# Kernel tuning notes

Hardware: AMD Instinct MI355X
Metric: run time of the kernel (lower is better)

## Reference

```python
import jax, jax.numpy as jnp
import numpy as np

B, S, D = 4, 2048, 512
H, DQK, DV = 6, 64, 64
PROJ = (DQK + DQK + DV) * H  # 1152
EPS = 1e-5


def setup_inputs() -> dict:
    key = jax.random.key(0)
    ks = jax.random.split(key, 5)
    sc = 0.05
    return {
        "x": jax.random.normal(ks[0], (B, S, D), jnp.float32),
        "Wp": jax.random.normal(ks[1], (PROJ, D), jnp.float32) * sc,
        "bp": jax.random.normal(ks[2], (PROJ,), jnp.float32) * sc,
        "Wo": jax.random.normal(ks[3], (D, H * DV), jnp.float32) * sc,
        "bo": jax.random.normal(ks[4], (D,), jnp.float32) * sc,
        "gamma": jnp.ones((D,), jnp.float32),
        "beta": jnp.zeros((D,), jnp.float32),
    }


def reference(x, Wp, bp, Wo, bo, gamma, beta):
    b, s, d = x.shape
    # 1x1 Conv1d projection == pointwise linear: [b,s,d] @ [d,proj] -> [b,s,proj]
    proj = jnp.einsum("bsd,pd->bsp", x, Wp) + bp
    q, k, v = proj[..., : H * DQK], proj[..., H * DQK : 2 * H * DQK], proj[..., 2 * H * DQK :]
    # split heads -> [b,h,s,depth]
    q = q.reshape(b, s, H, DQK).transpose(0, 2, 1, 3)
    k = k.reshape(b, s, H, DQK).transpose(0, 2, 1, 3)
    v = v.reshape(b, s, H, DV).transpose(0, 2, 1, 3)
    scores = jnp.einsum("bhqd,bhkd->bhqk", q, k) / jnp.sqrt(jnp.float32(DQK))
    attn = jax.nn.softmax(scores, axis=-1)  # softmax over kv axis
    out = jnp.einsum("bhqk,bhkd->bhqd", attn, v)
    # concat heads -> [b,s,h*dv]
    concat = out.transpose(0, 2, 1, 3).reshape(b, s, H * DV)
    y = jnp.einsum("bsf,df->bsd", concat, Wo) + bo
    z = x + y
    mu = jnp.mean(z, axis=-1, keepdims=True)
    var = jnp.mean(jnp.square(z - mu), axis=-1, keepdims=True)
    return (z - mu) / jnp.sqrt(var + EPS) * gamma + beta
```

## Files before the change

kernel.cpp:

```cpp
#include <hip/hip_runtime.h>

typedef __bf16 bf16;
typedef __bf16 bf16x8 __attribute__((ext_vector_type(8)));
typedef __bf16 bf16x4 __attribute__((ext_vector_type(4)));
typedef float  f32x4  __attribute__((ext_vector_type(4)));

#define BB 4
#define SS 2048
#define DD 512
#define HH 6
#define DH 64
#define PROJ 1152
#define FF 384
#define LDK 72

__device__ __forceinline__ bool probe_fp32(const unsigned* p) {
    return p[0] == 0x3F800000u;
}

struct CvtSrcs { const void* s[7]; };

#define CB0 524288
#define CB1 598016
#define CB2 622592
#define CB3 622736
#define CB4 622800
#define CB5 622864
#define CB6 622928

__global__ __launch_bounds__(256) void cvt_all_kernel(
    CvtSrcs srcs, bf16* __restrict__ dst, const unsigned* __restrict__ probe)
{
    const int t = blockIdx.x * 256 + threadIdx.x;
    if (t >= CB6) return;
    int seg, base;
    if      (t < CB0) { seg = 0; base = 0;   }
    else if (t < CB1) { seg = 1; base = CB0; }
    else if (t < CB2) { seg = 2; base = CB1; }
    else if (t < CB3) { seg = 3; base = CB2; }
    else if (t < CB4) { seg = 4; base = CB3; }
    else if (t < CB5) { seg = 5; base = CB4; }
    else              { seg = 6; base = CB5; }
    const int li = (t - base) * 8;
    if (probe_fp32(probe)) {
        const float* s = (const float*)srcs.s[seg] + li;
        bf16x8 o;
#pragma unroll
        for (int j = 0; j < 8; ++j) o[j] = (bf16)s[j];
        *(bf16x8*)&dst[(size_t)t * 8] = o;
    } else {
        *(bf16x8*)&dst[(size_t)t * 8] =
            *(const bf16x8*)((const bf16*)srcs.s[seg] + li);
    }
}

template<int MERGE, int STORE_F32>
__global__ __launch_bounds__(256) void gemm_bt_kernel(
    const bf16* __restrict__ A, const float* __restrict__ lpart,
    const bf16* __restrict__ B, const bf16* __restrict__ bias,
    void* __restrict__ Cout, int M, int N, int K)
{
    __shared__ __attribute__((aligned(16))) bf16 sA[128 * LDK];
    __shared__ __attribute__((aligned(16))) bf16 sB[128 * LDK];

    const int tid  = threadIdx.x;
    const int lane = tid & 63;
    const int wave = tid >> 6;
    const int wm = (wave >> 1) * 64;
    const int wn = (wave & 1) * 64;
    const int l15 = lane & 15;
    const int quad = lane >> 4;
    const int bm = blockIdx.x * 128;
    const int bn = blockIdx.y * 128;
    const int KT = K / 64;

    int srow[4], scol;
    scol = (tid & 7) << 3;
#pragma unroll
    for (int j = 0; j < 4; ++j) srow[j] = (j * 256 + tid) >> 3;

    const bf16* pA[4]; const bf16* pB[4];
    const float* pl0[4];
#pragma unroll
    for (int j = 0; j < 4; ++j) {
        if (MERGE) {
            int row = bm + srow[j];
            int b = row >> 11, q = row & (SS - 1);
            pA[j]  = A + ((size_t)(b * HH) * SS + q) * DH + scol;
            pl0[j] = lpart + (size_t)(b * HH) * SS + q;
        } else {
            pA[j] = A + (size_t)(bm + srow[j]) * K + scol;
        }
        pB[j] = B + (size_t)(bn + srow[j]) * K + scol;
    }

    bf16x8 ar0[4], ar1[4], br[4];
    float li0[4], li1[4];
#pragma unroll
    for (int j = 0; j < 4; ++j) {
        ar0[j] = *(const bf16x8*)pA[j];
        if (MERGE) {
            ar1[j] = *(const bf16x8*)(pA[j] + (size_t)BB * HH * SS * DH);
            li0[j] = pl0[j][0];
            li1[j] = pl0[j][(size_t)BB * HH * SS];
        }
        br[j] = *(const bf16x8*)pB[j];
    }

    const f32x4 fzero = {0.f, 0.f, 0.f, 0.f};
    f32x4 acc[4][4];
#pragma unroll
    for (int mi = 0; mi < 4; ++mi)
#pragma unroll
        for (int ni = 0; ni < 4; ++ni) acc[mi][ni] = fzero;

    for (int kt = 0; kt < KT; ++kt) {
        __syncthreads();
#pragma unroll
        for (int j = 0; j < 4; ++j) {
            if (MERGE) {
                float inv = 1.f / (li0[j] + li1[j]);
                bf16x8 m;
#pragma unroll
                for (int e = 0; e < 8; ++e)
                    m[e] = (bf16)(((float)ar0[j][e] + (float)ar1[j][e]) * inv);
                *(bf16x8*)&sA[srow[j] * LDK + scol] = m;
            } else {
                *(bf16x8*)&sA[srow[j] * LDK + scol] = ar0[j];
            }
            *(bf16x8*)&sB[srow[j] * LDK + scol] = br[j];
        }
        __syncthreads();

        if (kt + 1 < KT) {
#pragma unroll
            for (int j = 0; j < 4; ++j) {
                if (MERGE) {
                    pA[j]  += (size_t)SS * DH;
                    pl0[j] += SS;
                    ar0[j] = *(const bf16x8*)pA[j];
                    ar1[j] = *(const bf16x8*)(pA[j] + (size_t)BB * HH * SS * DH);
                    li0[j] = pl0[j][0];
                    li1[j] = pl0[j][(size_t)BB * HH * SS];
                } else {
                    pA[j] += 64;
                    ar0[j] = *(const bf16x8*)pA[j];
                }
                pB[j] += 64;
                br[j] = *(const bf16x8*)pB[j];
            }
        }

#pragma unroll
        for (int kk = 0; kk < 2; ++kk) {
            bf16x8 af[4], bfr[4];
#pragma unroll
            for (int i = 0; i < 4; ++i) {
                af[i]  = *(const bf16x8*)&sA[(wm + i * 16 + l15) * LDK + kk * 32 + quad * 8];
                bfr[i] = *(const bf16x8*)&sB[(wn + i * 16 + l15) * LDK + kk * 32 + quad * 8];
            }
#pragma unroll
            for (int mi = 0; mi < 4; ++mi)
#pragma unroll
                for (int ni = 0; ni < 4; ++ni)
                    acc[mi][ni] = __builtin_amdgcn_mfma_f32_16x16x32_bf16(
                        af[mi], bfr[ni], acc[mi][ni], 0, 0, 0);
        }
    }

#pragma unroll
    for (int mi = 0; mi < 4; ++mi) {
        int row = bm + wm + mi * 16 + quad * 4;
#pragma unroll
        for (int ni = 0; ni < 4; ++ni) {
            int col = bn + wn + ni * 16 + l15;
            float bv = (float)bias[col];
#pragma unroll
            for (int r = 0; r < 4; ++r) {
                float v = acc[mi][ni][r] + bv;
                if (STORE_F32) ((float*)Cout)[(size_t)(row + r) * N + col] = v;
                else           ((bf16*)Cout)[(size_t)(row + r) * N + col] = (bf16)v;
            }
        }
    }
}

__global__ __launch_bounds__(256) void vt_kernel(
    const bf16* __restrict__ proj, bf16* __restrict__ Vt)
{
    __shared__ __attribute__((aligned(16))) bf16 lt[64 * LDK];

    const int tid = threadIdx.x;
    const int s0 = blockIdx.x * 64;
    const int bh = blockIdx.y;
    const int b = bh / HH, h = bh % HH;

#pragma unroll
    for (int i = 0; i < 2; ++i) {
        int vid = i * 256 + tid;
        int sl = vid >> 3;
        int dc = (vid & 7) << 3;
        bf16x8 v = *(const bf16x8*)&proj[
            (size_t)(b * SS + s0 + sl) * PROJ + 2 * HH * DH + h * DH + dc];
#pragma unroll
        for (int j = 0; j < 8; ++j) {
            int d = dc + j;
            lt[d * LDK + (sl ^ (((d >> 3) & 3) * 8))] = v[j];
        }
    }
    __syncthreads();

#pragma unroll
    for (int i = 0; i < 2; ++i) {
        int vid = i * 256 + tid;
        int d = vid >> 3;
        int sc = (vid & 7) << 3;
        bf16x8 v = *(const bf16x8*)&lt[d * LDK + (sc ^ (((d >> 3) & 3) * 8))];
        *(bf16x8*)&Vt[(size_t)bh * DH * SS + (size_t)d * SS + s0 + sc] = v;
    }
}

__global__ __launch_bounds__(256) void attn_kernel(
    const bf16* __restrict__ proj, const bf16* __restrict__ Vt,
    bf16* __restrict__ Opart, float* __restrict__ lpart)
{
    __shared__ __attribute__((aligned(16))) bf16 sK [64 * LDK];
    __shared__ __attribute__((aligned(16))) bf16 sVt[64 * LDK];
    __shared__ __attribute__((aligned(16))) bf16 sP [4 * 32 * LDK];

    const int tid  = threadIdx.x;
    const int lane = tid & 63;
    const int wave = tid >> 6;
    const int l15  = lane & 15;
    const int quad = lane >> 4;

    const int bh = blockIdx.y;
    const int b = bh / HH, h = bh % HH;
    const int q0 = blockIdx.x * 128;
    const int kz = blockIdx.z;
    const bf16* base = proj + (size_t)b * SS * PROJ;
    const bf16* vtb  = Vt + (size_t)bh * DH * SS;

    const int sr = tid >> 3;
    const int sc = (tid & 7) << 3;

    bf16x8 qf[2][2];
#pragma unroll
    for (int g = 0; g < 2; ++g) {
        const int qrow = q0 + wave * 32 + g * 16 + l15;
#pragma unroll
        for (int ks = 0; ks < 2; ++ks) {
            qf[ks][g] = *(const bf16x8*)&base[
                (size_t)qrow * PROJ + h * DH + ks * 32 + quad * 8];
#pragma unroll
            for (int j = 0; j < 8; ++j)
                qf[ks][g][j] = (bf16)((float)qf[ks][g][j] * 0.125f);
        }
    }

    const f32x4 fzero = {0.f, 0.f, 0.f, 0.f};
    float l_part[2] = {0.f, 0.f};
    f32x4 oacc[2][4];
#pragma unroll
    for (int g = 0; g < 2; ++g)
#pragma unroll
        for (int fi = 0; fi < 4; ++fi) oacc[g][fi] = fzero;

    bf16* pw = &sP[wave * 32 * LDK];

    const int kt0 = kz * (SS / 128);
    const int kt1 = kt0 + SS / 128;

    bf16x8 kreg[2], vreg[2];
#pragma unroll
    for (int i = 0; i < 2; ++i) {
        int r = i * 32 + sr;
        kreg[i] = *(const bf16x8*)&base[(size_t)(kt0 * 64 + r) * PROJ + HH * DH + h * DH + sc];
        vreg[i] = *(const bf16x8*)&vtb[(size_t)r * SS + kt0 * 64 + sc];
    }

    for (int kt = kt0; kt < kt1; ++kt) {
        __syncthreads();
#pragma unroll
        for (int i = 0; i < 2; ++i) {
            int r = i * 32 + sr;
            *(bf16x8*)&sK [r * LDK + sc] = kreg[i];
            *(bf16x8*)&sVt[r * LDK + sc] = vreg[i];
        }
        __syncthreads();
        if (kt + 1 < kt1) {
#pragma unroll
            for (int i = 0; i < 2; ++i) {
                int r = i * 32 + sr;
                kreg[i] = *(const bf16x8*)&base[
                    (size_t)((kt + 1) * 64 + r) * PROJ + HH * DH + h * DH + sc];
                vreg[i] = *(const bf16x8*)&vtb[(size_t)r * SS + (kt + 1) * 64 + sc];
            }
        }

        f32x4 st[2][4];
#pragma unroll
        for (int g = 0; g < 2; ++g)
#pragma unroll
            for (int mi = 0; mi < 4; ++mi) st[g][mi] = fzero;
#pragma unroll
        for (int ks = 0; ks < 2; ++ks)
#pragma unroll
            for (int mi = 0; mi < 4; ++mi) {
                bf16x8 af = *(const bf16x8*)&sK[(mi * 16 + l15) * LDK + ks * 32 + quad * 8];
#pragma unroll
                for (int g = 0; g < 2; ++g)
                    st[g][mi] = __builtin_amdgcn_mfma_f32_16x16x32_bf16(
                        af, qf[ks][g], st[g][mi], 0, 0, 0);
            }

#pragma unroll
        for (int g = 0; g < 2; ++g)
#pragma unroll
            for (int mi = 0; mi < 4; ++mi)
#pragma unroll
                for (int r = 0; r < 4; ++r) {
                    st[g][mi][r] = __expf(st[g][mi][r]);
                    l_part[g] += st[g][mi][r];
                }

#pragma unroll
        for (int g = 0; g < 2; ++g)
#pragma unroll
            for (int mi = 0; mi < 4; ++mi) {
                bf16x4 p4;
#pragma unroll
                for (int r = 0; r < 4; ++r) p4[r] = (bf16)st[g][mi][r];
                *(bf16x4*)&pw[(g * 16 + l15) * LDK + mi * 16 + quad * 4] = p4;
            }

#pragma unroll
        for (int ks = 0; ks < 2; ++ks) {
            bf16x8 bfrag[2];
#pragma unroll
            for (int g = 0; g < 2; ++g)
                bfrag[g] = *(const bf16x8*)&pw[(g * 16 + l15) * LDK + ks * 32 + quad * 8];
#pragma unroll
            for (int fi = 0; fi < 4; ++fi) {
                bf16x8 af = *(const bf16x8*)&sVt[(fi * 16 + l15) * LDK + ks * 32 + quad * 8];
#pragma unroll
                for (int g = 0; g < 2; ++g)
                    oacc[g][fi] = __builtin_amdgcn_mfma_f32_16x16x32_bf16(
                        af, bfrag[g], oacc[g][fi], 0, 0, 0);
            }
        }
    }

#pragma unroll
    for (int g = 0; g < 2; ++g) {
        l_part[g] += __shfl_xor(l_part[g], 16);
        l_part[g] += __shfl_xor(l_part[g], 32);
    }

    const size_t zoff = (size_t)(kz * BB * HH + bh) * SS;
#pragma unroll
    for (int g = 0; g < 2; ++g) {
        const int qg = q0 + wave * 32 + g * 16 + l15;
        bf16* orow = Opart + (zoff + qg) * DH;
#pragma unroll
        for (int fi = 0; fi < 4; ++fi) {
            bf16x4 o4;
#pragma unroll
            for (int r = 0; r < 4; ++r) o4[r] = (bf16)oacc[g][fi][r];
            *(bf16x4*)&orow[fi * 16 + quad * 4] = o4;
        }
    }
    if (lane < 16) {
#pragma unroll
        for (int g = 0; g < 2; ++g)
            lpart[zoff + q0 + wave * 32 + g * 16 + lane] = l_part[g];
    }
}

__global__ __launch_bounds__(256) void ln_kernel(
    const void* __restrict__ xr, const float* __restrict__ y,
    const bf16* __restrict__ gamma, const bf16* __restrict__ beta,
    void* __restrict__ out, const unsigned* __restrict__ probe)
{
    const bool f32 = probe_fp32(probe);
    const int lane = threadIdx.x & 63;
    const int wave = threadIdx.x >> 6;
    const int row = blockIdx.x * 4 + wave;
    const size_t off = (size_t)row * DD + lane * 8;

    float z[8];
    if (f32) {
        const float* xf = (const float*)xr;
#pragma unroll
        for (int j = 0; j < 8; ++j) z[j] = xf[off + j];
    } else {
        bf16x8 xv = *(const bf16x8*)&((const bf16*)xr)[off];
#pragma unroll
        for (int j = 0; j < 8; ++j) z[j] = (float)xv[j];
    }
    f32x4 y0 = *(const f32x4*)&y[off];
    f32x4 y1 = *(const f32x4*)&y[off + 4];
#pragma unroll
    for (int j = 0; j < 4; ++j) { z[j] += y0[j]; z[j + 4] += y1[j]; }

    float s = 0.f;
#pragma unroll
    for (int j = 0; j < 8; ++j) s += z[j];
#pragma unroll
    for (int m = 1; m < 64; m <<= 1) s += __shfl_xor(s, m);
    float mu = s * (1.f / DD);
    float s2 = 0.f;
#pragma unroll
    for (int j = 0; j < 8; ++j) { float d = z[j] - mu; s2 += d * d; }
#pragma unroll
    for (int m = 1; m < 64; m <<= 1) s2 += __shfl_xor(s2, m);
    float rs = rsqrtf(s2 * (1.f / DD) + 1e-5f);

    bf16x8 gm = *(const bf16x8*)&gamma[lane * 8];
    bf16x8 be = *(const bf16x8*)&beta[lane * 8];
    if (f32) {
        f32x4 o0, o1;
#pragma unroll
        for (int j = 0; j < 4; ++j) {
            o0[j] = (z[j]     - mu) * rs * (float)gm[j]     + (float)be[j];
            o1[j] = (z[j + 4] - mu) * rs * (float)gm[j + 4] + (float)be[j + 4];
        }
        *(f32x4*)&((float*)out)[off]     = o0;
        *(f32x4*)&((float*)out)[off + 4] = o1;
    } else {
        bf16x8 o;
#pragma unroll
        for (int j = 0; j < 8; ++j)
            o[j] = (bf16)((z[j] - mu) * rs * (float)gm[j] + (float)be[j]);
        *(bf16x8*)&((bf16*)out)[off] = o;
    }
}

extern "C" void kernel_launch(void* const* d_in, const int* in_sizes, int n_in,
                              void* d_out, int out_size, void* d_ws, size_t ws_size,
                              hipStream_t stream)
{
    const unsigned* probe = (const unsigned*)d_in[5];

    char* ws = (char*)d_ws;
    size_t o = 0;
    bf16* xb   = (bf16*)(ws + o); o += (size_t)BB * SS * DD * 2;
    bf16* Wpb  = (bf16*)(ws + o); o += (size_t)PROJ * DD * 2;
    bf16* Wob  = (bf16*)(ws + o); o += (size_t)DD * FF * 2;
    bf16* bpb  = (bf16*)(ws + o); o += PROJ * 2;
    bf16* bob  = (bf16*)(ws + o); o += DD * 2;
    bf16* gb   = (bf16*)(ws + o); o += DD * 2;
    bf16* bb   = (bf16*)(ws + o); o += DD * 2;
    bf16* proj = (bf16*)(ws + o); o += (size_t)BB * SS * PROJ * 2;
    bf16* vtbuf  = (bf16*)(ws + o); o += (size_t)BB * HH * DH * SS * 2;
    bf16* Opart  = (bf16*)(ws + o); o += (size_t)2 * BB * HH * SS * DH * 2;
    float* lpart = (float*)(ws + o); o += (size_t)2 * BB * HH * SS * 4;
    float* ybuf = (float*)proj;

    CvtSrcs srcs;
    srcs.s[0] = d_in[0]; srcs.s[1] = d_in[1]; srcs.s[2] = d_in[3];
    srcs.s[3] = d_in[2]; srcs.s[4] = d_in[4]; srcs.s[5] = d_in[5];
    srcs.s[6] = d_in[6];
    cvt_all_kernel<<<(CB6 + 255) / 256, 256, 0, stream>>>(srcs, xb, probe);

    gemm_bt_kernel<0, 0><<<dim3((BB * SS) / 128, PROJ / 128), 256, 0, stream>>>(
        xb, nullptr, Wpb, bpb, proj, BB * SS, PROJ, DD);
    vt_kernel<<<dim3(SS / 64, BB * HH), 256, 0, stream>>>(proj, vtbuf);
    attn_kernel<<<dim3(SS / 128, BB * HH, 2), 256, 0, stream>>>(
        proj, vtbuf, Opart, lpart);
    gemm_bt_kernel<1, 1><<<dim3((BB * SS) / 128, DD / 128), 256, 0, stream>>>(
        Opart, lpart, Wob, bob, ybuf, BB * SS, DD, FF);
    ln_kernel<<<dim3((BB * SS) / 4), 256, 0, stream>>>(
        d_in[0], ybuf, gb, bb, d_out, probe);
}
```

Measured before the change: 166.7 us.

## Double-buffer global prefetch two tiles ahead and use exp2 with folded log2e scale

Both the GEMM and attention kernels now keep two register sets of prefetched tiles and issue global loads two k-steps ahead, so more load latency is hidden behind MFMA work. The attention softmax folds log2(e) into the Q scale and uses the hardware exp2 instruction. It also accumulates row sums as vector adds rather than scalar chains. This costs extra registers, which may lower occupancy, and assumes the k-tile count is even.

```diff
diff --git a/kernel.cpp b/kernel.cpp
--- a/kernel.cpp
+++ b/kernel.cpp
@@ -16,6 +16,14 @@
 
 __device__ __forceinline__ bool probe_fp32(const unsigned* p) {
     return p[0] == 0x3F800000u;
+}
+
+__device__ __forceinline__ float fast_exp2(float x) {
+#if __has_builtin(__builtin_amdgcn_exp2f)
+    return __builtin_amdgcn_exp2f(x);
+#else
+    return __expf(x * 0.69314718f);
+#endif
 }
 
 struct CvtSrcs { const void* s[7]; };
@@ -74,8 +82,8 @@
     const int bn = blockIdx.y * 128;
     const int KT = K / 64;
 
-    int srow[4], scol;
-    scol = (tid & 7) << 3;
+    int srow[4];
+    const int scol = (tid & 7) << 3;
 #pragma unroll
     for (int j = 0; j < 4; ++j) srow[j] = (j * 256 + tid) >> 3;
 
@@ -94,18 +102,29 @@
         pB[j] = B + (size_t)(bn + srow[j]) * K + scol;
     }
 
-    bf16x8 ar0[4], ar1[4], br[4];
-    float li0[4], li1[4];
-#pragma unroll
-    for (int j = 0; j < 4; ++j) {
-        ar0[j] = *(const bf16x8*)pA[j];
-        if (MERGE) {
-            ar1[j] = *(const bf16x8*)(pA[j] + (size_t)BB * HH * SS * DH);
-            li0[j] = pl0[j][0];
-            li1[j] = pl0[j][(size_t)BB * HH * SS];
-        }
-        br[j] = *(const bf16x8*)pB[j];
-    }
+    auto loadAB = [&](bf16x8 (&a0)[4], bf16x8 (&a1)[4],
+                      float (&l0)[4], float (&l1)[4], bf16x8 (&b)[4]) {
+#pragma unroll
+        for (int j = 0; j < 4; ++j) {
+            a0[j] = *(const bf16x8*)pA[j];
+            if (MERGE) {
+                a1[j] = *(const bf16x8*)(pA[j] + (size_t)BB * HH * SS * DH);
+                l0[j] = pl0[j][0];
+                l1[j] = pl0[j][(size_t)BB * HH * SS];
+                pA[j]  += (size_t)SS * DH;
+                pl0[j] += SS;
+            } else {
+                pA[j] += 64;
+            }
+            b[j] = *(const bf16x8*)pB[j];
+            pB[j] += 64;
+        }
+    };
+
+    bf16x8 a0A[4], a1A[4], bA[4]; float l0A[4], l1A[4];
+    bf16x8 a0B[4], a1B[4], bB[4]; float l0B[4], l1B[4];
+    loadAB(a0A, a1A, l0A, l1A, bA);
+    loadAB(a0B, a1B, l0B, l1B, bB);
 
     const f32x4 fzero = {0.f, 0.f, 0.f, 0.f};
     f32x4 acc[4][4];
@@ -114,42 +133,25 @@
 #pragma unroll
         for (int ni = 0; ni < 4; ++ni) acc[mi][ni] = fzero;
 
-    for (int kt = 0; kt < KT; ++kt) {
+    auto step = [&](int kt, bf16x8 (&a0)[4], bf16x8 (&a1)[4],
+                    float (&l0)[4], float (&l1)[4], bf16x8 (&b)[4]) {
         __syncthreads();
 #pragma unroll
         for (int j = 0; j < 4; ++j) {
             if (MERGE) {
-                float inv = 1.f / (li0[j] + li1[j]);
+                float inv = 1.f / (l0[j] + l1[j]);
                 bf16x8 m;
 #pragma unroll
                 for (int e = 0; e < 8; ++e)
-                    m[e] = (bf16)(((float)ar0[j][e] + (float)ar1[j][e]) * inv);
+                    m[e] = (bf16)(((float)a0[j][e] + (float)a1[j][e]) * inv);
                 *(bf16x8*)&sA[srow[j] * LDK + scol] = m;
             } else {
-                *(bf16x8*)&sA[srow[j] * LDK + scol] = ar0[j];
-            }
-            *(bf16x8*)&sB[srow[j] * LDK + scol] = br[j];
+                *(bf16x8*)&sA[srow[j] * LDK + scol] = a0[j];
+            }
+            *(bf16x8*)&sB[srow[j] * LDK + scol] = b[j];
         }
         __syncthreads();
-
-        if (kt + 1 < KT) {
-#pragma unroll
-            for (int j = 0; j < 4; ++j) {
-                if (MERGE) {
-                    pA[j]  += (size_t)SS * DH;
-                    pl0[j] += SS;
-                    ar0[j] = *(const bf16x8*)pA[j];
-                    ar1[j] = *(const bf16x8*)(pA[j] + (size_t)BB * HH * SS * DH);
-                    li0[j] = pl0[j][0];
-                    li1[j] = pl0[j][(size_t)BB * HH * SS];
-                } else {
-                    pA[j] += 64;
-                    ar0[j] = *(const bf16x8*)pA[j];
-                }
-                pB[j] += 64;
-                br[j] = *(const bf16x8*)pB[j];
-            }
-        }
+        if (kt + 2 < KT) loadAB(a0, a1, l0, l1, b);
 
 #pragma unroll
         for (int kk = 0; kk < 2; ++kk) {
@@ -166,6 +168,11 @@
                     acc[mi][ni] = __builtin_amdgcn_mfma_f32_16x16x32_bf16(
                         af[mi], bfr[ni], acc[mi][ni], 0, 0, 0);
         }
+    };
+
+    for (int kt = 0; kt < KT; kt += 2) {
+        step(kt,     a0A, a1A, l0A, l1A, bA);
+        step(kt + 1, a0B, a1B, l0B, l1B, bB);
     }
 
 #pragma unroll
@@ -244,6 +251,7 @@
     const int sr = tid >> 3;
     const int sc = (tid & 7) << 3;
 
+    const float QS = 0.18033688f;
     bf16x8 qf[2][2];
 #pragma unroll
     for (int g = 0; g < 2; ++g) {
@@ -254,12 +262,12 @@
                 (size_t)qrow * PROJ + h * DH + ks * 32 + quad * 8];
 #pragma unroll
             for (int j = 0; j < 8; ++j)
-                qf[ks][g][j] = (bf16)((float)qf[ks][g][j] * 0.125f);
+                qf[ks][g][j] = (bf16)((float)qf[ks][g][j] * QS);
         }
     }
 
     const f32x4 fzero = {0.f, 0.f, 0.f, 0.f};
-    float l_part[2] = {0.f, 0.f};
+    f32x4 lacc[2] = {fzero, fzero};
     f32x4 oacc[2][4];
 #pragma unroll
     for (int g = 0; g < 2; ++g)
@@ -271,58 +279,61 @@
     const int kt0 = kz * (SS / 128);
     const int kt1 = kt0 + SS / 128;
 
-    bf16x8 kreg[2], vreg[2];
+    const bf16* pk[2]; const bf16* pv[2];
 #pragma unroll
     for (int i = 0; i < 2; ++i) {
         int r = i * 32 + sr;
-        kreg[i] = *(const bf16x8*)&base[(size_t)(kt0 * 64 + r) * PROJ + HH * DH + h * DH + sc];
-        vreg[i] = *(const bf16x8*)&vtb[(size_t)r * SS + kt0 * 64 + sc];
-    }
-
-    for (int kt = kt0; kt < kt1; ++kt) {
+        pk[i] = &base[(size_t)(kt0 * 64 + r) * PROJ + HH * DH + h * DH + sc];
+        pv[i] = &vtb[(size_t)r * SS + kt0 * 64 + sc];
+    }
+    auto loadKV = [&](bf16x8 (&kr)[2], bf16x8 (&vr)[2]) {
+#pragma unroll
+        for (int i = 0; i < 2; ++i) {
+            kr[i] = *(const bf16x8*)pk[i];
+            vr[i] = *(const bf16x8*)pv[i];
+            pk[i] += (size_t)64 * PROJ;
+            pv[i] += 64;
+        }
+    };
+
+    bf16x8 kA[2], vA[2], kB[2], vB[2];
+    loadKV(kA, vA);
+    loadKV(kB, vB);
+
+    auto tile = [&](int kt, bf16x8 (&kr)[2], bf16x8 (&vr)[2]) {
         __syncthreads();
 #pragma unroll
         for (int i = 0; i < 2; ++i) {
             int r = i * 32 + sr;
-            *(bf16x8*)&sK [r * LDK + sc] = kreg[i];
-            *(bf16x8*)&sVt[r * LDK + sc] = vreg[i];
+            *(bf16x8*)&sK [r * LDK + sc] = kr[i];
+            *(bf16x8*)&sVt[r * LDK + sc] = vr[i];
         }
         __syncthreads();
-        if (kt + 1 < kt1) {
-#pragma unroll
-            for (int i = 0; i < 2; ++i) {
-                int r = i * 32 + sr;
-                kreg[i] = *(const bf16x8*)&base[
-                    (size_t)((kt + 1) * 64 + r) * PROJ + HH * DH + h * DH + sc];
-                vreg[i] = *(const bf16x8*)&vtb[(size_t)r * SS + (kt + 1) * 64 + sc];
-            }
-        }
+        if (kt + 2 < kt1) loadKV(kr, vr);
 
         f32x4 st[2][4];
 #pragma unroll
+        for (int mi = 0; mi < 4; ++mi) {
+            bf16x8 af0 = *(const bf16x8*)&sK[(mi * 16 + l15) * LDK + quad * 8];
+            bf16x8 af1 = *(const bf16x8*)&sK[(mi * 16 + l15) * LDK + 32 + quad * 8];
+#pragma unroll
+            for (int g = 0; g < 2; ++g) {
+                st[g][mi] = __builtin_amdgcn_mfma_f32_16x16x32_bf16(
+                    af0, qf[0][g], fzero, 0, 0, 0);
+                st[g][mi] = __builtin_amdgcn_mfma_f32_16x16x32_bf16(
+                    af1, qf[1][g], st[g][mi], 0, 0, 0);
+            }
+        }
+
+#pragma unroll
         for (int g = 0; g < 2; ++g)
 #pragma unroll
-            for (int mi = 0; mi < 4; ++mi) st[g][mi] = fzero;
-#pragma unroll
-        for (int ks = 0; ks < 2; ++ks)
-#pragma unroll
             for (int mi = 0; mi < 4; ++mi) {
-                bf16x8 af = *(const bf16x8*)&sK[(mi * 16 + l15) * LDK + ks * 32 + quad * 8];
-#pragma unroll
-                for (int g = 0; g < 2; ++g)
-                    st[g][mi] = __builtin_amdgcn_mfma_f32_16x16x32_bf16(
-                        af, qf[ks][g], st[g][mi], 0, 0, 0);
-            }
-
-#pragma unroll
-        for (int g = 0; g < 2; ++g)
-#pragma unroll
-            for (int mi = 0; mi < 4; ++mi)
-#pragma unroll
-                for (int r = 0; r < 4; ++r) {
-                    st[g][mi][r] = __expf(st[g][mi][r]);
-                    l_part[g] += st[g][mi][r];
-                }
+#pragma unroll
+                for (int r = 0; r < 4; ++r)
+                    st[g][mi][r] = fast_exp2(st[g][mi][r]);
+                lacc[g] += st[g][mi];
+            }
 
 #pragma unroll
         for (int g = 0; g < 2; ++g)
@@ -349,10 +360,17 @@
                         af, bfrag[g], oacc[g][fi], 0, 0, 0);
             }
         }
-    }
-
+    };
+
+    for (int kt = kt0; kt < kt1; kt += 2) {
+        tile(kt,     kA, vA);
+        tile(kt + 1, kB, vB);
+    }
+
+    float l_part[2];
 #pragma unroll
     for (int g = 0; g < 2; ++g) {
+        l_part[g] = lacc[g][0] + lacc[g][1] + lacc[g][2] + lacc[g][3];
         l_part[g] += __shfl_xor(l_part[g], 16);
         l_part[g] += __shfl_xor(l_part[g], 32);
     }
```

Result: no change. 167.5 us (+0.5%).
